# Kernel tuning notes

Hardware: AMD Instinct MI355X
Metric: run time of the kernel (lower is better)

## Reference

```python
import jax, jax.numpy as jnp
import numpy as np

N_NODES = 50000
N_EDGES = 640000
IN_CH = 32
OUT_CH = 64
H1 = 2 * IN_CH   # 64
H2 = 4 * IN_CH   # 128


def _sage_conv(x, src, dst, w_l, b_l, w_r, n_nodes):
    """PyG SAGEConv (mean aggr): out = mean_{j in N(i)} x_j @ w_l + b_l + x_i @ w_r."""
    msg = x[src]                                                  # [E, d] gather
    agg = jax.ops.segment_sum(msg, dst, num_segments=n_nodes)    # [N, d]
    cnt = jax.ops.segment_sum(jnp.ones_like(dst, x.dtype), dst, num_segments=n_nodes)
    mean = agg / jnp.maximum(cnt, 1.0)[:, None]                   # empty neighborhoods -> 0
    return mean @ w_l + b_l + x @ w_r


def setup_inputs() -> dict:
    key = jax.random.key(0)
    ks = jax.random.split(key, 9)
    x = jax.random.normal(ks[0], (N_NODES, IN_CH), dtype=jnp.float32)
    edge_index = jax.random.randint(ks[1], (2, N_EDGES), 0, N_NODES, dtype=jnp.int32)

    def glorot(k, shape):
        fan_in, fan_out = shape
        s = jnp.sqrt(6.0 / (fan_in + fan_out))
        return jax.random.uniform(k, shape, jnp.float32, -s, s)

    return {
        "x": x,
        "edge_index": edge_index,
        "w1_l": glorot(ks[2], (IN_CH, H1)), "b1": jnp.zeros((H1,), jnp.float32),
        "w1_r": glorot(ks[3], (IN_CH, H1)),
        "w2_l": glorot(ks[4], (H1, H2)), "b2": jnp.zeros((H2,), jnp.float32),
        "w2_r": glorot(ks[5], (H1, H2)),
        "w3_l": glorot(ks[6], (H2, OUT_CH)), "b3": jnp.zeros((OUT_CH,), jnp.float32),
        "w3_r": glorot(ks[7], (H2, OUT_CH)),
    }


def reference(x, edge_index, w1_l, b1, w1_r, w2_l, b2, w2_r, w3_l, b3, w3_r):
    n = x.shape[0]
    src, dst = edge_index[0], edge_index[1]
    h = jax.nn.relu(_sage_conv(x, src, dst, w1_l, b1, w1_r, n))
    h = jax.nn.relu(_sage_conv(h, src, dst, w2_l, b2, w2_r, n))
    return _sage_conv(h, src, dst, w3_l, b3, w3_r, n)
```

## Files before the change

### kernel.cpp

```cpp
#include <hip/hip_runtime.h>


typedef short bf8 __attribute__((ext_vector_type(8)));
typedef float f32x4 __attribute__((ext_vector_type(4)));

__device__ inline ushort bf16rn(float f) {
    unsigned u = __float_as_uint(f);
    return (ushort)((u + 0x7FFFu + ((u >> 16) & 1u)) >> 16);
}
__device__ inline float bf16tof(ushort h) {
    return __uint_as_float(((unsigned)h) << 16);
}
__device__ inline void split8(const float4 pa, const float4 pb, bf8& hi, bf8& lo) {
    const float v[8] = {pa.x, pa.y, pa.z, pa.w, pb.x, pb.y, pb.z, pb.w};
#pragma unroll
    for (int j = 0; j < 8; ++j) {
        const ushort h = bf16rn(v[j]);
        hi[j] = (short)h;
        lo[j] = (short)bf16rn(v[j] - bf16tof(h));
    }
}

__global__ __launch_bounds__(256) void prep_kernel(
    const float* __restrict__ x,
    const float* __restrict__ w1l, const float* __restrict__ w1r,
    const float* __restrict__ w2l, const float* __restrict__ w2r,
    const float* __restrict__ w3l, const float* __restrict__ w3r,
    ushort* __restrict__ wprep, int* __restrict__ cnt,
    ushort* __restrict__ xh, int nN, int nCntZero)
{
    const int g = blockIdx.x * 256 + threadIdx.x;
    const int n = gridDim.x * 256;
    for (int f = g; f < 9216; f += n) {
        int base, KCs, oc0, d0, wstride;
        const float *wa, *wb;
        if (f < 1024)      { base = 0;    KCs = 2; oc0 = 0;  wa = w1l; wb = w1r; d0 = 32;  wstride = 64;  }
        else if (f < 3072) { base = 1024; KCs = 4; oc0 = 0;  wa = w2l; wb = w2r; d0 = 64;  wstride = 128; }
        else if (f < 5120) { base = 3072; KCs = 4; oc0 = 64; wa = w2l; wb = w2r; d0 = 64;  wstride = 128; }
        else if (f < 7168) { base = 5120; KCs = 4; oc0 = 0;  wa = w3l; wb = w3l; d0 = 128; wstride = 64;  }
        else               { base = 7168; KCs = 4; oc0 = 0;  wa = w3r; wb = w3r; d0 = 128; wstride = 64;  }
        const int local = f - base;
        const int lane = local & 63;
        const int s = (local >> 6) & 1;
        const int kcct = local >> 7;
        const int kc = kcct % KCs;
        const int ct = kcct / KCs;
        const int col = oc0 + ct * 16 + (lane & 15);
        const int k0 = kc * 32 + (lane >> 4) * 8;
        ushort h8[8];
#pragma unroll
        for (int j = 0; j < 8; ++j) {
            const int k = k0 + j;
            const float* wr = (k < d0) ? (wa + (size_t)k * wstride)
                                       : (wb + (size_t)(k - d0) * wstride);
            const float v = wr[col];
            const ushort h = bf16rn(v);
            h8[j] = (s == 0) ? h : bf16rn(v - bf16tof(h));
        }
        *reinterpret_cast<int4*>(wprep + (size_t)f * 8) = *reinterpret_cast<const int4*>(h8);
    }
    for (int i = g; i < nCntZero / 4; i += n)
        reinterpret_cast<int4*>(cnt)[i] = make_int4(0, 0, 0, 0);
    const int nxv = nN * 4;
    for (int i = g; i < nxv; i += n) {
        const float4 a = reinterpret_cast<const float4*>(x)[i * 2 + 0];
        const float4 b = reinterpret_cast<const float4*>(x)[i * 2 + 1];
        const float v[8] = {a.x, a.y, a.z, a.w, b.x, b.y, b.z, b.w};
        bf8 h;
#pragma unroll
        for (int j = 0; j < 8; ++j) h[j] = (short)bf16rn(v[j]);
        reinterpret_cast<bf8*>(xh)[i] = h;
    }
}

__global__ __launch_bounds__(256) void count_kernel(const int* __restrict__ dst,
                                                    int* __restrict__ cnt,
                                                    int* __restrict__ pos, int nE) {
    int i = blockIdx.x * blockDim.x + threadIdx.x;
    int e0 = i * 4;
    if (e0 + 3 < nE) {
        int4 d = *reinterpret_cast<const int4*>(dst + e0);
        int4 p;
        p.x = atomicAdd(&cnt[d.x], 1);
        p.y = atomicAdd(&cnt[d.y], 1);
        p.z = atomicAdd(&cnt[d.z], 1);
        p.w = atomicAdd(&cnt[d.w], 1);
        *reinterpret_cast<int4*>(pos + e0) = p;
    } else {
        for (int e = e0; e < nE; ++e) pos[e] = atomicAdd(&cnt[dst[e]], 1);
    }
}

__global__ __launch_bounds__(256) void scan_blocks(const int* __restrict__ cnt,
                                                   int* __restrict__ rowptr,
                                                   int* __restrict__ partials, int nN) {
    __shared__ int wsum[4];
    const int t = threadIdx.x;
    const int lane = t & 63, wid = t >> 6;
    const int base = blockIdx.x * 1024 + t * 4;

    int4 v = make_int4(0, 0, 0, 0);
    if (base + 3 < nN) {
        v = *reinterpret_cast<const int4*>(cnt + base);
    } else {
        if (base + 0 < nN) v.x = cnt[base + 0];
        if (base + 1 < nN) v.y = cnt[base + 1];
        if (base + 2 < nN) v.z = cnt[base + 2];
        if (base + 3 < nN) v.w = cnt[base + 3];
    }
    const int s = v.x + v.y + v.z + v.w;

    int inc = s;
#pragma unroll
    for (int d = 1; d < 64; d <<= 1) {
        int u = __shfl_up(inc, d);
        if (lane >= d) inc += u;
    }
    if (lane == 63) wsum[wid] = inc;
    __syncthreads();
    int woff = 0;
#pragma unroll
    for (int w = 0; w < 4; ++w) woff += (w < wid) ? wsum[w] : 0;

    const int excl = woff + inc - s;
    int4 o;
    o.x = excl; o.y = excl + v.x; o.z = excl + v.x + v.y; o.w = excl + v.x + v.y + v.z;
    if (base + 3 < nN) {
        *reinterpret_cast<int4*>(rowptr + base) = o;
    } else {
        if (base + 0 < nN) rowptr[base + 0] = o.x;
        if (base + 1 < nN) rowptr[base + 1] = o.y;
        if (base + 2 < nN) rowptr[base + 2] = o.z;
        if (base + 3 < nN) rowptr[base + 3] = o.w;
    }
    if (t == 255) partials[blockIdx.x] = woff + inc;
}

__global__ __launch_bounds__(256) void scan_add(int* __restrict__ rowptr,
                                                const int* __restrict__ partials,
                                                int nN, int nE) {
    __shared__ int soff;
    const int t = threadIdx.x;
    if (t < 64) {
        int v = (t < blockIdx.x) ? partials[t] : 0;
#pragma unroll
        for (int d = 32; d >= 1; d >>= 1) v += __shfl_xor(v, d);
        if (t == 0) soff = v;
    }
    __syncthreads();
    const int off = soff;
    const int base = blockIdx.x * 1024 + t * 4;
    if (base + 3 < nN) {
        int4 v = *reinterpret_cast<int4*>(rowptr + base);
        v.x += off; v.y += off; v.z += off; v.w += off;
        *reinterpret_cast<int4*>(rowptr + base) = v;
    } else {
        if (base + 0 < nN) rowptr[base + 0] += off;
        if (base + 1 < nN) rowptr[base + 1] += off;
        if (base + 2 < nN) rowptr[base + 2] += off;
        if (base + 3 < nN) rowptr[base + 3] += off;
    }
    if (blockIdx.x == 0 && t == 0) rowptr[nN] = nE;
}

__global__ __launch_bounds__(256) void fill_kernel(const int* __restrict__ src,
                                                   const int* __restrict__ dst,
                                                   const int* __restrict__ pos,
                                                   const int* __restrict__ rowptr,
                                                   int* __restrict__ csr_src, int nE) {
    int i = blockIdx.x * blockDim.x + threadIdx.x;
    int e0 = i * 4;
    if (e0 + 3 < nE) {
        int4 s4 = *reinterpret_cast<const int4*>(src + e0);
        int4 d4 = *reinterpret_cast<const int4*>(dst + e0);
        int4 p4 = *reinterpret_cast<const int4*>(pos + e0);
        csr_src[rowptr[d4.x] + p4.x] = s4.x;
        csr_src[rowptr[d4.y] + p4.y] = s4.y;
        csr_src[rowptr[d4.z] + p4.z] = s4.z;
        csr_src[rowptr[d4.w] + p4.w] = s4.w;
    } else {
        for (int e = e0; e < nE; ++e)
            csr_src[rowptr[dst[e]] + pos[e]] = src[e];
    }
}

__global__ __launch_bounds__(256) void fused_layer1(
    const float* __restrict__ x, const ushort* __restrict__ xh,
    const int* __restrict__ rowptr, const int* __restrict__ csr_src,
    const ushort* __restrict__ wfrag, const float* __restrict__ b1,
    ushort* __restrict__ h1h, ushort* __restrict__ h1l, int nN)
{
    __shared__ float tile[64 * 36];
    __shared__ ushort wlds[1024 * 8];

    const int tid = threadIdx.x;
    const int node0 = blockIdx.x * 64;

    {
        const int4* wsrc = reinterpret_cast<const int4*>(wfrag);
        int4* wl = reinterpret_cast<int4*>(wlds);
        for (int i = tid; i < 1024; i += 256) wl[i] = wsrc[i];
    }
    {
        const int nl = tid >> 2;
        const int c = tid & 3;
        const int node = node0 + nl;
        float acc[8] = {0.f, 0.f, 0.f, 0.f, 0.f, 0.f, 0.f, 0.f};
        if (node < nN) {
            const int beg = rowptr[node], end = rowptr[node + 1];
            int e = beg;
            for (; e + 7 < end; e += 8) {
                int si[8];
#pragma unroll
                for (int j = 0; j < 8; ++j) si[j] = csr_src[e + j];
                bf8 v[8];
#pragma unroll
                for (int j = 0; j < 8; ++j)
                    v[j] = *reinterpret_cast<const bf8*>(xh + (size_t)si[j] * 32 + c * 8);
#pragma unroll
                for (int k = 0; k < 8; ++k)
#pragma unroll
                    for (int j = 0; j < 8; ++j) acc[k] += bf16tof((ushort)v[j][k]);
            }
            for (; e < end; ++e) {
                bf8 v = *reinterpret_cast<const bf8*>(xh + (size_t)csr_src[e] * 32 + c * 8);
#pragma unroll
                for (int k = 0; k < 8; ++k) acc[k] += bf16tof((ushort)v[k]);
            }
            const float sc = 1.0f / (float)max(end - beg, 1);
#pragma unroll
            for (int k = 0; k < 8; ++k) acc[k] *= sc;
        }
        *reinterpret_cast<float4*>(&tile[nl * 36 + c * 8 + 0]) =
            make_float4(acc[0], acc[1], acc[2], acc[3]);
        *reinterpret_cast<float4*>(&tile[nl * 36 + c * 8 + 4]) =
            make_float4(acc[4], acc[5], acc[6], acc[7]);
    }
    __syncthreads();

    const int w = tid >> 6, lane = tid & 63;
    const int rloc = w * 16 + (lane & 15);
    const int arow = min(node0 + rloc, nN - 1);
    const int kg = lane >> 4;
    bf8 ahi[2], alo[2];
    {
        const float* tp = &tile[rloc * 36 + kg * 8];
        split8(*reinterpret_cast<const float4*>(tp),
               *reinterpret_cast<const float4*>(tp + 4), ahi[0], alo[0]);
    }
    {
        const float* rp = x + (size_t)arow * 32 + kg * 8;
        split8(*reinterpret_cast<const float4*>(rp),
               *reinterpret_cast<const float4*>(rp + 4), ahi[1], alo[1]);
    }
    const bf8* bgl = reinterpret_cast<const bf8*>(wlds);
#pragma unroll
    for (int ct = 0; ct < 4; ++ct) {
        f32x4 acc = {0.f, 0.f, 0.f, 0.f};
#pragma unroll
        for (int kc = 0; kc < 2; ++kc) {
            const bf8 bhi = bgl[((ct * 2 + kc) * 2 + 0) * 64 + lane];
            const bf8 blo = bgl[((ct * 2 + kc) * 2 + 1) * 64 + lane];
            acc = __builtin_amdgcn_mfma_f32_16x16x32_bf16(ahi[kc], bhi, acc, 0, 0, 0);
            acc = __builtin_amdgcn_mfma_f32_16x16x32_bf16(ahi[kc], blo, acc, 0, 0, 0);
            acc = __builtin_amdgcn_mfma_f32_16x16x32_bf16(alo[kc], bhi, acc, 0, 0, 0);
        }
        const int col = ct * 16 + (lane & 15);
        const float bv = b1[col];
#pragma unroll
        for (int r = 0; r < 4; ++r) {
            const int node = node0 + w * 16 + (lane >> 4) * 4 + r;
            if (node < nN) {
                const float o = fmaxf(acc[r] + bv, 0.f);
                const ushort hi = bf16rn(o);
                h1h[(size_t)node * 64 + col] = hi;
                h1l[(size_t)node * 64 + col] = bf16rn(o - bf16tof(hi));
            }
        }
    }
}

__global__ __launch_bounds__(256) void fused_layer2(
    const ushort* __restrict__ h1h, const ushort* __restrict__ h1l,
    const int* __restrict__ rowptr, const int* __restrict__ csr_src,
    const ushort* __restrict__ wfrag, const float* __restrict__ b2,
    float* __restrict__ h2, int nN)
{
    __shared__ float tile[64 * 68];

    const int tid = threadIdx.x;
    const int node0 = blockIdx.x * 64;

    {
        const int c = tid & 7;
        const int nl0 = tid >> 3;
#pragma unroll
        for (int p = 0; p < 2; ++p) {
            const int nl = p * 32 + nl0;
            const int node = node0 + nl;
            float acc[8] = {0.f, 0.f, 0.f, 0.f, 0.f, 0.f, 0.f, 0.f};
            if (node < nN) {
                const int beg = rowptr[node], end = rowptr[node + 1];
                int e = beg;
                for (; e + 7 < end; e += 8) {
                    int si[8];
#pragma unroll
                    for (int j = 0; j < 8; ++j) si[j] = csr_src[e + j];
                    bf8 v[8];
#pragma unroll
                    for (int j = 0; j < 8; ++j)
                        v[j] = *reinterpret_cast<const bf8*>(h1h + (size_t)si[j] * 64 + c * 8);
#pragma unroll
                    for (int k = 0; k < 8; ++k)
#pragma unroll
                        for (int j = 0; j < 8; ++j) acc[k] += bf16tof((ushort)v[j][k]);
                }
                for (; e < end; ++e) {
                    bf8 v = *reinterpret_cast<const bf8*>(h1h + (size_t)csr_src[e] * 64 + c * 8);
#pragma unroll
                    for (int k = 0; k < 8; ++k) acc[k] += bf16tof((ushort)v[k]);
                }
                const float sc = 1.0f / (float)max(end - beg, 1);
#pragma unroll
                for (int k = 0; k < 8; ++k) acc[k] *= sc;
            }
            *reinterpret_cast<float4*>(&tile[nl * 68 + c * 8 + 0]) =
                make_float4(acc[0], acc[1], acc[2], acc[3]);
            *reinterpret_cast<float4*>(&tile[nl * 68 + c * 8 + 4]) =
                make_float4(acc[4], acc[5], acc[6], acc[7]);
        }
    }
    __syncthreads();

    const int w = tid >> 6, lane = tid & 63;
    const int rloc = w * 16 + (lane & 15);
    const int arow = min(node0 + rloc, nN - 1);
    const int kg = lane >> 4;
    bf8 ahi[4], alo[4];
#pragma unroll
    for (int kc = 0; kc < 2; ++kc) {
        const float* tp = &tile[rloc * 68 + kc * 32 + kg * 8];
        split8(*reinterpret_cast<const float4*>(tp),
               *reinterpret_cast<const float4*>(tp + 4), ahi[kc], alo[kc]);
    }
#pragma unroll
    for (int kc = 2; kc < 4; ++kc) {
        const size_t off = (size_t)arow * 64 + (kc - 2) * 32 + kg * 8;
        ahi[kc] = *reinterpret_cast<const bf8*>(h1h + off);
        alo[kc] = *reinterpret_cast<const bf8*>(h1l + off);
    }
#pragma unroll
    for (int ct = 0; ct < 8; ++ct) {
        const int sec = ct >> 2, ctl = ct & 3;
        const bf8* bgl = reinterpret_cast<const bf8*>(wfrag) + sec * 2048;
        f32x4 acc = {0.f, 0.f, 0.f, 0.f};
#pragma unroll
        for (int kc = 0; kc < 4; ++kc) {
            const bf8 bhi = bgl[((ctl * 4 + kc) * 2 + 0) * 64 + lane];
            const bf8 blo = bgl[((ctl * 4 + kc) * 2 + 1) * 64 + lane];
            acc = __builtin_amdgcn_mfma_f32_16x16x32_bf16(ahi[kc], bhi, acc, 0, 0, 0);
            acc = __builtin_amdgcn_mfma_f32_16x16x32_bf16(ahi[kc], blo, acc, 0, 0, 0);
            acc = __builtin_amdgcn_mfma_f32_16x16x32_bf16(alo[kc], bhi, acc, 0, 0, 0);
        }
        const int col = ct * 16 + (lane & 15);
        const float bv = b2[col];
#pragma unroll
        for (int r = 0; r < 4; ++r) {
            const int node = node0 + w * 16 + (lane >> 4) * 4 + r;
            if (node < nN) h2[(size_t)node * 128 + col] = fmaxf(acc[r] + bv, 0.f);
        }
    }
}

__global__ __launch_bounds__(256) void mfma_dual(
    const float* __restrict__ h2, const ushort* __restrict__ wfrag,
    const float* __restrict__ b3, ushort* __restrict__ t3h,
    float* __restrict__ r3, int nN)
{
    __shared__ ushort wlds[2048 * 8];

    const int tid = threadIdx.x;
    const int sel = blockIdx.y;
    {
        const int4* wsrc = reinterpret_cast<const int4*>(wfrag) + (size_t)sel * 2048;
        int4* wl = reinterpret_cast<int4*>(wlds);
        for (int i = tid; i < 2048; i += 256) wl[i] = wsrc[i];
    }
    __syncthreads();

    const int w = tid >> 6, lane = tid & 63;
    const int node0 = blockIdx.x * 64;
    const int arow = min(node0 + w * 16 + (lane & 15), nN - 1);
    const int kg = lane >> 4;
    bf8 ahi[4], alo[4];
#pragma unroll
    for (int kc = 0; kc < 4; ++kc) {
        const float* rp = h2 + (size_t)arow * 128 + kc * 32 + kg * 8;
        split8(*reinterpret_cast<const float4*>(rp),
               *reinterpret_cast<const float4*>(rp + 4), ahi[kc], alo[kc]);
    }
    const bf8* bgl = reinterpret_cast<const bf8*>(wlds);
#pragma unroll
    for (int ct = 0; ct < 4; ++ct) {
        f32x4 acc = {0.f, 0.f, 0.f, 0.f};
#pragma unroll
        for (int kc = 0; kc < 4; ++kc) {
            const bf8 bhi = bgl[((ct * 4 + kc) * 2 + 0) * 64 + lane];
            const bf8 blo = bgl[((ct * 4 + kc) * 2 + 1) * 64 + lane];
            acc = __builtin_amdgcn_mfma_f32_16x16x32_bf16(ahi[kc], bhi, acc, 0, 0, 0);
            acc = __builtin_amdgcn_mfma_f32_16x16x32_bf16(ahi[kc], blo, acc, 0, 0, 0);
            acc = __builtin_amdgcn_mfma_f32_16x16x32_bf16(alo[kc], bhi, acc, 0, 0, 0);
        }
        const int col = ct * 16 + (lane & 15);
#pragma unroll
        for (int r = 0; r < 4; ++r) {
            const int node = node0 + w * 16 + (lane >> 4) * 4 + r;
            if (node < nN) {
                if (sel) r3[(size_t)node * 64 + col] = acc[r] + b3[col];
                else     t3h[(size_t)node * 64 + col] = bf16rn(acc[r]);
            }
        }
    }
}

__global__ __launch_bounds__(256) void final_gather(
    const ushort* __restrict__ t3h, const int* __restrict__ rowptr,
    const int* __restrict__ csr_src, const float* __restrict__ r3,
    float* __restrict__ dout, int nN)
{
    const int tid = threadIdx.x;
    const int node = blockIdx.x * 32 + (tid >> 3);
    const int c = tid & 7;
    if (node >= nN) return;
    const int beg = rowptr[node], end = rowptr[node + 1];
    float acc[8] = {0.f, 0.f, 0.f, 0.f, 0.f, 0.f, 0.f, 0.f};
    int e = beg;
    for (; e + 7 < end; e += 8) {
        int si[8];
#pragma unroll
        for (int j = 0; j < 8; ++j) si[j] = csr_src[e + j];
        bf8 v[8];
#pragma unroll
        for (int j = 0; j < 8; ++j)
            v[j] = *reinterpret_cast<const bf8*>(t3h + (size_t)si[j] * 64 + c * 8);
#pragma unroll
        for (int k = 0; k < 8; ++k)
#pragma unroll
            for (int j = 0; j < 8; ++j) acc[k] += bf16tof((ushort)v[j][k]);
    }
    for (; e < end; ++e) {
        bf8 v = *reinterpret_cast<const bf8*>(t3h + (size_t)csr_src[e] * 64 + c * 8);
#pragma unroll
        for (int k = 0; k < 8; ++k) acc[k] += bf16tof((ushort)v[k]);
    }
    const float sc = 1.0f / (float)max(end - beg, 1);
    const float4 a0 = reinterpret_cast<const float4*>(r3)[(size_t)node * 16 + c * 2 + 0];
    const float4 a1 = reinterpret_cast<const float4*>(r3)[(size_t)node * 16 + c * 2 + 1];
    float4 o0, o1;
    o0.x = fmaf(acc[0], sc, a0.x); o0.y = fmaf(acc[1], sc, a0.y);
    o0.z = fmaf(acc[2], sc, a0.z); o0.w = fmaf(acc[3], sc, a0.w);
    o1.x = fmaf(acc[4], sc, a1.x); o1.y = fmaf(acc[5], sc, a1.y);
    o1.z = fmaf(acc[6], sc, a1.z); o1.w = fmaf(acc[7], sc, a1.w);
    reinterpret_cast<float4*>(dout)[(size_t)node * 16 + c * 2 + 0] = o0;
    reinterpret_cast<float4*>(dout)[(size_t)node * 16 + c * 2 + 1] = o1;
}

extern "C" void kernel_launch(void* const* d_in, const int* in_sizes, int n_in,
                              void* d_out, int out_size, void* d_ws, size_t ws_size,
                              hipStream_t stream) {
    const float* x   = (const float*)d_in[0];
    const int*   ei  = (const int*)d_in[1];
    const float* w1l = (const float*)d_in[2];
    const float* b1  = (const float*)d_in[3];
    const float* w1r = (const float*)d_in[4];
    const float* w2l = (const float*)d_in[5];
    const float* b2  = (const float*)d_in[6];
    const float* w2r = (const float*)d_in[7];
    const float* w3l = (const float*)d_in[8];
    const float* b3  = (const float*)d_in[9];
    const float* w3r = (const float*)d_in[10];

    const int nN = in_sizes[0] / 32;
    const int nE = in_sizes[1] / 2;
    const int* src = ei;
    const int* dst = ei + nE;
    const int nB = (nN + 1023) / 1024;
    const int nCntZero = (nN + 63) & ~63;

    char* ws = (char*)d_ws;
    size_t o = 0;
    auto alloc = [&](size_t nbytes) {
        char* p = ws + o;
        o += (nbytes + 255) & ~(size_t)255;
        return p;
    };
    int*    cnt      = (int*)alloc((size_t)nCntZero * sizeof(int));
    int*    pos      = (int*)alloc((size_t)nE * sizeof(int));
    int*    partials = (int*)alloc(64 * sizeof(int));
    int*    rowptr   = (int*)alloc(((size_t)nN + 1) * sizeof(int));
    int*    csr_src  = (int*)alloc((size_t)nE * sizeof(int));
    ushort* wprep    = (ushort*)alloc((size_t)9216 * 8 * sizeof(ushort));
    ushort* xh       = (ushort*)alloc((size_t)nN * 32 * sizeof(ushort));
    ushort* h1h      = (ushort*)alloc((size_t)nN * 64 * sizeof(ushort));
    ushort* h1l      = (ushort*)alloc((size_t)nN * 64 * sizeof(ushort));
    float*  h2       = (float*)alloc((size_t)nN * 128 * sizeof(float));
    ushort* t3h      = (ushort*)alloc((size_t)nN * 64 * sizeof(ushort));
    float*  r3       = (float*)alloc((size_t)nN * 64 * sizeof(float));

    prep_kernel<<<784, 256, 0, stream>>>(x, w1l, w1r, w2l, w2r, w3l, w3r,
                                         wprep, cnt, xh, nN, nCntZero);
    count_kernel<<<(nE / 4 + 255) / 256, 256, 0, stream>>>(dst, cnt, pos, nE);
    scan_blocks<<<nB, 256, 0, stream>>>(cnt, rowptr, partials, nN);
    scan_add<<<nB, 256, 0, stream>>>(rowptr, partials, nN, nE);
    fill_kernel<<<(nE / 4 + 255) / 256, 256, 0, stream>>>(src, dst, pos, rowptr, csr_src, nE);

    const int xblk = (nN + 63) / 64;

    fused_layer1<<<xblk, 256, 0, stream>>>(x, xh, rowptr, csr_src, wprep, b1, h1h, h1l, nN);
    fused_layer2<<<xblk, 256, 0, stream>>>(h1h, h1l, rowptr, csr_src,
                                           wprep + (size_t)1024 * 8, b2, h2, nN);
    mfma_dual<<<dim3(xblk, 2), 256, 0, stream>>>(h2, wprep + (size_t)5120 * 8, b3, t3h, r3, nN);
    final_gather<<<(nN + 31) / 32, 256, 0, stream>>>(t3h, rowptr, csr_src, r3, (float*)d_out, nN);
}
```

Baseline: 140.7 us.

## Use 16-bit CSR indices, pre-split h2 to bf16 pairs, merge mfma_dual grid

Edge position and CSR source index buffers are narrowed from int32 to uint16. This halves the index traffic read by the three neighbor-gather kernels and by the CSR build, but it only holds while node count and per-node degree stay below 65536. Layer 2 now writes its output as bf16 hi/lo halves instead of fp32, so the last MFMA kernel no longer has to split values. mfma_dual now computes both the neighbor and root projections in one block per tile, reading weight fragments from global memory instead of LDS, so the A-operand rows are loaded once rather than twice.

```diff
diff --git a/kernel.cpp b/kernel.cpp
--- a/kernel.cpp
+++ b/kernel.cpp
@@ -75,19 +75,19 @@
 
 __global__ __launch_bounds__(256) void count_kernel(const int* __restrict__ dst,
                                                     int* __restrict__ cnt,
-                                                    int* __restrict__ pos, int nE) {
+                                                    ushort* __restrict__ pos, int nE) {
     int i = blockIdx.x * blockDim.x + threadIdx.x;
     int e0 = i * 4;
     if (e0 + 3 < nE) {
         int4 d = *reinterpret_cast<const int4*>(dst + e0);
-        int4 p;
-        p.x = atomicAdd(&cnt[d.x], 1);
-        p.y = atomicAdd(&cnt[d.y], 1);
-        p.z = atomicAdd(&cnt[d.z], 1);
-        p.w = atomicAdd(&cnt[d.w], 1);
-        *reinterpret_cast<int4*>(pos + e0) = p;
+        ushort4 p;
+        p.x = (ushort)atomicAdd(&cnt[d.x], 1);
+        p.y = (ushort)atomicAdd(&cnt[d.y], 1);
+        p.z = (ushort)atomicAdd(&cnt[d.z], 1);
+        p.w = (ushort)atomicAdd(&cnt[d.w], 1);
+        *reinterpret_cast<ushort4*>(pos + e0) = p;
     } else {
-        for (int e = e0; e < nE; ++e) pos[e] = atomicAdd(&cnt[dst[e]], 1);
+        for (int e = e0; e < nE; ++e) pos[e] = (ushort)atomicAdd(&cnt[dst[e]], 1);
     }
 }
 
@@ -165,28 +165,28 @@
 
 __global__ __launch_bounds__(256) void fill_kernel(const int* __restrict__ src,
                                                    const int* __restrict__ dst,
-                                                   const int* __restrict__ pos,
+                                                   const ushort* __restrict__ pos,
                                                    const int* __restrict__ rowptr,
-                                                   int* __restrict__ csr_src, int nE) {
+                                                   ushort* __restrict__ csr_src, int nE) {
     int i = blockIdx.x * blockDim.x + threadIdx.x;
     int e0 = i * 4;
     if (e0 + 3 < nE) {
         int4 s4 = *reinterpret_cast<const int4*>(src + e0);
         int4 d4 = *reinterpret_cast<const int4*>(dst + e0);
-        int4 p4 = *reinterpret_cast<const int4*>(pos + e0);
-        csr_src[rowptr[d4.x] + p4.x] = s4.x;
-        csr_src[rowptr[d4.y] + p4.y] = s4.y;
-        csr_src[rowptr[d4.z] + p4.z] = s4.z;
-        csr_src[rowptr[d4.w] + p4.w] = s4.w;
+        ushort4 p4 = *reinterpret_cast<const ushort4*>(pos + e0);
+        csr_src[rowptr[d4.x] + p4.x] = (ushort)s4.x;
+        csr_src[rowptr[d4.y] + p4.y] = (ushort)s4.y;
+        csr_src[rowptr[d4.z] + p4.z] = (ushort)s4.z;
+        csr_src[rowptr[d4.w] + p4.w] = (ushort)s4.w;
     } else {
         for (int e = e0; e < nE; ++e)
-            csr_src[rowptr[dst[e]] + pos[e]] = src[e];
+            csr_src[rowptr[dst[e]] + pos[e]] = (ushort)src[e];
     }
 }
 
 __global__ __launch_bounds__(256) void fused_layer1(
     const float* __restrict__ x, const ushort* __restrict__ xh,
-    const int* __restrict__ rowptr, const int* __restrict__ csr_src,
+    const int* __restrict__ rowptr, const ushort* __restrict__ csr_src,
     const ushort* __restrict__ wfrag, const float* __restrict__ b1,
     ushort* __restrict__ h1h, ushort* __restrict__ h1l, int nN)
 {
@@ -282,9 +282,9 @@
 
 __global__ __launch_bounds__(256) void fused_layer2(
     const ushort* __restrict__ h1h, const ushort* __restrict__ h1l,
-    const int* __restrict__ rowptr, const int* __restrict__ csr_src,
+    const int* __restrict__ rowptr, const ushort* __restrict__ csr_src,
     const ushort* __restrict__ wfrag, const float* __restrict__ b2,
-    float* __restrict__ h2, int nN)
+    ushort* __restrict__ h2h, ushort* __restrict__ h2l, int nN)
 {
     __shared__ float tile[64 * 68];
 
@@ -367,57 +367,56 @@
 #pragma unroll
         for (int r = 0; r < 4; ++r) {
             const int node = node0 + w * 16 + (lane >> 4) * 4 + r;
-            if (node < nN) h2[(size_t)node * 128 + col] = fmaxf(acc[r] + bv, 0.f);
+            if (node < nN) {
+                const float o = fmaxf(acc[r] + bv, 0.f);
+                const ushort hi = bf16rn(o);
+                h2h[(size_t)node * 128 + col] = hi;
+                h2l[(size_t)node * 128 + col] = bf16rn(o - bf16tof(hi));
+            }
         }
     }
 }
 
 __global__ __launch_bounds__(256) void mfma_dual(
-    const float* __restrict__ h2, const ushort* __restrict__ wfrag,
-    const float* __restrict__ b3, ushort* __restrict__ t3h,
-    float* __restrict__ r3, int nN)
+    const ushort* __restrict__ h2h, const ushort* __restrict__ h2l,
+    const ushort* __restrict__ wfrag, const float* __restrict__ b3,
+    ushort* __restrict__ t3h, float* __restrict__ r3, int nN)
 {
-    __shared__ ushort wlds[2048 * 8];
-
     const int tid = threadIdx.x;
-    const int sel = blockIdx.y;
-    {
-        const int4* wsrc = reinterpret_cast<const int4*>(wfrag) + (size_t)sel * 2048;
-        int4* wl = reinterpret_cast<int4*>(wlds);
-        for (int i = tid; i < 2048; i += 256) wl[i] = wsrc[i];
-    }
-    __syncthreads();
-
     const int w = tid >> 6, lane = tid & 63;
     const int node0 = blockIdx.x * 64;
     const int arow = min(node0 + w * 16 + (lane & 15), nN - 1);
     const int kg = lane >> 4;
+
     bf8 ahi[4], alo[4];
 #pragma unroll
     for (int kc = 0; kc < 4; ++kc) {
-        const float* rp = h2 + (size_t)arow * 128 + kc * 32 + kg * 8;
-        split8(*reinterpret_cast<const float4*>(rp),
-               *reinterpret_cast<const float4*>(rp + 4), ahi[kc], alo[kc]);
-    }
-    const bf8* bgl = reinterpret_cast<const bf8*>(wlds);
-#pragma unroll
-    for (int ct = 0; ct < 4; ++ct) {
-        f32x4 acc = {0.f, 0.f, 0.f, 0.f};
-#pragma unroll
-        for (int kc = 0; kc < 4; ++kc) {
-            const bf8 bhi = bgl[((ct * 4 + kc) * 2 + 0) * 64 + lane];
-            const bf8 blo = bgl[((ct * 4 + kc) * 2 + 1) * 64 + lane];
-            acc = __builtin_amdgcn_mfma_f32_16x16x32_bf16(ahi[kc], bhi, acc, 0, 0, 0);
-            acc = __builtin_amdgcn_mfma_f32_16x16x32_bf16(ahi[kc], blo, acc, 0, 0, 0);
-            acc = __builtin_amdgcn_mfma_f32_16x16x32_bf16(alo[kc], bhi, acc, 0, 0, 0);
-        }
-        const int col = ct * 16 + (lane & 15);
-#pragma unroll
-        for (int r = 0; r < 4; ++r) {
-            const int node = node0 + w * 16 + (lane >> 4) * 4 + r;
-            if (node < nN) {
-                if (sel) r3[(size_t)node * 64 + col] = acc[r] + b3[col];
-                else     t3h[(size_t)node * 64 + col] = bf16rn(acc[r]);
+        const size_t off = (size_t)arow * 128 + kc * 32 + kg * 8;
+        ahi[kc] = *reinterpret_cast<const bf8*>(h2h + off);
+        alo[kc] = *reinterpret_cast<const bf8*>(h2l + off);
+    }
+#pragma unroll
+    for (int sel = 0; sel < 2; ++sel) {
+        const bf8* bgl = reinterpret_cast<const bf8*>(wfrag) + sel * 2048;
+#pragma unroll
+        for (int ct = 0; ct < 4; ++ct) {
+            f32x4 acc = {0.f, 0.f, 0.f, 0.f};
+#pragma unroll
+            for (int kc = 0; kc < 4; ++kc) {
+                const bf8 bhi = bgl[((ct * 4 + kc) * 2 + 0) * 64 + lane];
+                const bf8 blo = bgl[((ct * 4 + kc) * 2 + 1) * 64 + lane];
+                acc = __builtin_amdgcn_mfma_f32_16x16x32_bf16(ahi[kc], bhi, acc, 0, 0, 0);
+                acc = __builtin_amdgcn_mfma_f32_16x16x32_bf16(ahi[kc], blo, acc, 0, 0, 0);
+                acc = __builtin_amdgcn_mfma_f32_16x16x32_bf16(alo[kc], bhi, acc, 0, 0, 0);
+            }
+            const int col = ct * 16 + (lane & 15);
+#pragma unroll
+            for (int r = 0; r < 4; ++r) {
+                const int node = node0 + w * 16 + (lane >> 4) * 4 + r;
+                if (node < nN) {
+                    if (sel) r3[(size_t)node * 64 + col] = acc[r] + b3[col];
+                    else     t3h[(size_t)node * 64 + col] = bf16rn(acc[r]);
+                }
             }
         }
     }
@@ -425,7 +424,7 @@
 
 __global__ __launch_bounds__(256) void final_gather(
     const ushort* __restrict__ t3h, const int* __restrict__ rowptr,
-    const int* __restrict__ csr_src, const float* __restrict__ r3,
+    const ushort* __restrict__ csr_src, const float* __restrict__ r3,
     float* __restrict__ dout, int nN)
 {
     const int tid = threadIdx.x;
@@ -495,15 +494,16 @@
         return p;
     };
     int*    cnt      = (int*)alloc((size_t)nCntZero * sizeof(int));
-    int*    pos      = (int*)alloc((size_t)nE * sizeof(int));
+    ushort* pos      = (ushort*)alloc((size_t)nE * sizeof(ushort));
     int*    partials = (int*)alloc(64 * sizeof(int));
     int*    rowptr   = (int*)alloc(((size_t)nN + 1) * sizeof(int));
-    int*    csr_src  = (int*)alloc((size_t)nE * sizeof(int));
+    ushort* csr_src  = (ushort*)alloc((size_t)nE * sizeof(ushort));
     ushort* wprep    = (ushort*)alloc((size_t)9216 * 8 * sizeof(ushort));
     ushort* xh       = (ushort*)alloc((size_t)nN * 32 * sizeof(ushort));
     ushort* h1h      = (ushort*)alloc((size_t)nN * 64 * sizeof(ushort));
     ushort* h1l      = (ushort*)alloc((size_t)nN * 64 * sizeof(ushort));
-    float*  h2       = (float*)alloc((size_t)nN * 128 * sizeof(float));
+    ushort* h2h      = (ushort*)alloc((size_t)nN * 128 * sizeof(ushort));
+    ushort* h2l      = (ushort*)alloc((size_t)nN * 128 * sizeof(ushort));
     ushort* t3h      = (ushort*)alloc((size_t)nN * 64 * sizeof(ushort));
     float*  r3       = (float*)alloc((size_t)nN * 64 * sizeof(float));
 
@@ -518,7 +518,7 @@
 
     fused_layer1<<<xblk, 256, 0, stream>>>(x, xh, rowptr, csr_src, wprep, b1, h1h, h1l, nN);
     fused_layer2<<<xblk, 256, 0, stream>>>(h1h, h1l, rowptr, csr_src,
-                                           wprep + (size_t)1024 * 8, b2, h2, nN);
-    mfma_dual<<<dim3(xblk, 2), 256, 0, stream>>>(h2, wprep + (size_t)5120 * 8, b3, t3h, r3, nN);
+                                           wprep + (size_t)1024 * 8, b2, h2h, h2l, nN);
+    mfma_dual<<<xblk, 256, 0, stream>>>(h2h, h2l, wprep + (size_t)5120 * 8, b3, t3h, r3, nN);
     final_gather<<<(nN + 31) / 32, 256, 0, stream>>>(t3h, rowptr, csr_src, r3, (float*)d_out, nN);
 }
```

After: 141.1 us. Within noise of the previous version (+0.2%).
